# Performance work log

Hardware: AMD Instinct MI355X
Metric: run time of the kernel (lower is better)

The kernel has to match this reference:

```python
import jax, jax.numpy as jnp
import numpy as np


def setup_inputs() -> dict:
    key = jax.random.key(0)
    k1, k2 = jax.random.split(key)
    N, C, H, W = 32, 1, 768, 1024
    inp = jax.random.normal(k1, (N, C, H, W), dtype=jnp.float32)
    # target values in {0,1,2}: 0=neg, 1=pos, 2=ignore
    tgt = jax.random.randint(k2, (N, C, H, W), 0, 3).astype(jnp.float32)
    return {"input": inp, "target": tgt}


def reference(input, target):
    # Flatten (NCHW -> NHWC -> flat); order is irrelevant for a mean reduction,
    # but we mirror the original transpose/view for faithfulness.
    x = jnp.transpose(input, (0, 2, 3, 1)).reshape(-1)
    t = jnp.transpose(target, (0, 2, 3, 1)).reshape(-1)

    pos = t == 1.0
    neg = t == 0.0
    pos_num = jnp.sum(pos).astype(x.dtype)
    neg_num = jnp.sum(neg).astype(x.dtype)
    sum_num = pos_num + neg_num

    # weight: neg_num/sum for positives, pos_num/sum for negatives, 0 for ignore (t>1)
    w = jnp.where(pos, neg_num / sum_num, jnp.where(neg, pos_num / sum_num, 0.0))

    # stable BCE-with-logits: max(x,0) - x*t + log1p(exp(-|x|))
    bce = jnp.maximum(x, 0.0) - x * t + jnp.log1p(jnp.exp(-jnp.abs(x)))
    return jnp.mean(w * bce)
```

## Files before the change

kernel.cpp:

```cpp
#include <hip/hip_runtime.h>


#define GRID1 2048
#define BLOCK 256

__device__ __forceinline__ void do_elem(float xv, float tv,
                                        float& cp, float& cn,
                                        float& sp, float& sn) {
  float a = fabsf(xv);
  float e = __expf(-a);
  float l = __logf(1.0f + e);
  float c = fmaxf(xv, 0.f) + l;
  bool pos = (tv == 1.0f);
  bool neg = (tv == 0.0f);
  cp += pos ? 1.0f : 0.0f;
  cn += neg ? 1.0f : 0.0f;
  sp += pos ? (c - xv) : 0.0f;
  sn += neg ? c : 0.0f;
}

__device__ __forceinline__ void do_vec4(float4 xv, float4 tv,
                                        float& cp, float& cn,
                                        float& sp, float& sn) {
  do_elem(xv.x, tv.x, cp, cn, sp, sn);
  do_elem(xv.y, tv.y, cp, cn, sp, sn);
  do_elem(xv.z, tv.z, cp, cn, sp, sn);
  do_elem(xv.w, tv.w, cp, cn, sp, sn);
}

__global__ __launch_bounds__(BLOCK, 8) void edge_loss_stage1(
    const float* __restrict__ x, const float* __restrict__ t,
    float* __restrict__ partials, long long n) {
  long long tid = (long long)blockIdx.x * BLOCK + threadIdx.x;
  long long S = (long long)gridDim.x * BLOCK;
  long long n4 = n >> 2;

  float cp = 0.f, cn = 0.f, sp = 0.f, sn = 0.f;

  const float4* __restrict__ x4 = (const float4*)x;
  const float4* __restrict__ t4 = (const float4*)t;

  long long i = tid;
  if (i < n4) {
    float4 xa = x4[i];
    float4 ta = t4[i];
    long long nxt = i + S;
    while (nxt < n4) {
      float4 xb = x4[nxt];
      float4 tb = t4[nxt];
      do_vec4(xa, ta, cp, cn, sp, sn);
      xa = xb;
      ta = tb;
      nxt += S;
    }
    do_vec4(xa, ta, cp, cn, sp, sn);
  }
  for (long long j = (n4 << 2) + tid; j < n; j += S) {
    do_elem(x[j], t[j], cp, cn, sp, sn);
  }

  #pragma unroll
  for (int off = 32; off > 0; off >>= 1) {
    cp += __shfl_down(cp, off, 64);
    cn += __shfl_down(cn, off, 64);
    sp += __shfl_down(sp, off, 64);
    sn += __shfl_down(sn, off, 64);
  }

  __shared__ float s_cp[4], s_cn[4], s_sp[4], s_sn[4];
  int lane = threadIdx.x & 63;
  int wave = threadIdx.x >> 6;
  if (lane == 0) { s_cp[wave] = cp; s_cn[wave] = cn; s_sp[wave] = sp; s_sn[wave] = sn; }
  __syncthreads();
  if (threadIdx.x == 0) {
    float tcp = 0.f, tcn = 0.f, tsp = 0.f, tsn = 0.f;
    #pragma unroll
    for (int k = 0; k < 4; ++k) { tcp += s_cp[k]; tcn += s_cn[k]; tsp += s_sp[k]; tsn += s_sn[k]; }
    int G = gridDim.x;
    partials[0 * G + blockIdx.x] = tcp;
    partials[1 * G + blockIdx.x] = tcn;
    partials[2 * G + blockIdx.x] = tsp;
    partials[3 * G + blockIdx.x] = tsn;
  }
}

__global__ __launch_bounds__(BLOCK) void edge_loss_stage2(
    const float* __restrict__ partials, float* __restrict__ out,
    int G, double inv_n) {
  double acc[4] = {0.0, 0.0, 0.0, 0.0};
  for (int i = threadIdx.x; i < G; i += BLOCK) {
    #pragma unroll
    for (int c = 0; c < 4; ++c) acc[c] += (double)partials[c * G + i];
  }
  #pragma unroll
  for (int off = 32; off > 0; off >>= 1) {
    #pragma unroll
    for (int c = 0; c < 4; ++c) acc[c] += __shfl_down(acc[c], off, 64);
  }
  __shared__ double s_acc[4][4];
  int lane = threadIdx.x & 63;
  int wave = threadIdx.x >> 6;
  if (lane == 0) {
    #pragma unroll
    for (int c = 0; c < 4; ++c) s_acc[wave][c] = acc[c];
  }
  __syncthreads();
  if (threadIdx.x == 0) {
    double pos = 0, neg = 0, spos = 0, sneg = 0;
    #pragma unroll
    for (int w = 0; w < 4; ++w) {
      pos += s_acc[w][0]; neg += s_acc[w][1];
      spos += s_acc[w][2]; sneg += s_acc[w][3];
    }
    double s = pos + neg;
    out[0] = (float)((neg * spos + pos * sneg) / s * inv_n);
  }
}

extern "C" void kernel_launch(void* const* d_in, const int* in_sizes, int n_in,
                              void* d_out, int out_size, void* d_ws, size_t ws_size,
                              hipStream_t stream) {
  const float* x = (const float*)d_in[0];
  const float* t = (const float*)d_in[1];
  long long n = (long long)in_sizes[0];
  float* partials = (float*)d_ws;

  edge_loss_stage1<<<GRID1, BLOCK, 0, stream>>>(x, t, partials, n);
  edge_loss_stage2<<<1, BLOCK, 0, stream>>>(partials, (float*)d_out,
                                            GRID1, 1.0 / (double)n);
}
```

Measured before the change: 215.0 us.

## Stream inputs through LDS with async global_load_lds double buffering

The register-prefetch grid-stride loop is replaced by direct global-to-LDS DMA loads (global_load_lds, 16 bytes per lane) into a per-wave double buffer, with s_waitcnt on vmcnt gating each stage. The goal is to keep loads in flight without holding them in VGPRs and so hide memory latency in this bandwidth-bound reduction. It adds LDS traffic, 16 KB of shared memory per block that may limit occupancy, and relies on hand-coded waitcnt encodings whose correctness depends on the target ISA.

Measured after the change: 216.8 us. Within noise of the previous version (+0.8%).

```diff
diff --git a/kernel.cpp b/kernel.cpp
--- a/kernel.cpp
+++ b/kernel.cpp
@@ -3,6 +3,15 @@
 
 #define GRID1 2048
 #define BLOCK 256
+
+#define WAITCNT_VM2 0x0F72
+#define WAITCNT_VM0 0x0F70
+
+__device__ __forceinline__ void dma16(const float4* g, float4* l) {
+  __builtin_amdgcn_global_load_lds(
+      (const __attribute__((address_space(1))) void*)g,
+      (__attribute__((address_space(3))) void*)l, 16, 0, 0);
+}
 
 __device__ __forceinline__ void do_elem(float xv, float tv,
                                         float& cp, float& cn,
@@ -31,31 +40,52 @@
 __global__ __launch_bounds__(BLOCK, 8) void edge_loss_stage1(
     const float* __restrict__ x, const float* __restrict__ t,
     float* __restrict__ partials, long long n) {
-  long long tid = (long long)blockIdx.x * BLOCK + threadIdx.x;
+  __shared__ float4 lds[2][2][BLOCK];
+
+  long long idx0 = (long long)blockIdx.x * BLOCK + threadIdx.x;
   long long S = (long long)gridDim.x * BLOCK;
   long long n4 = n >> 2;
+  long long niter = n4 / S;
 
-  float cp = 0.f, cn = 0.f, sp = 0.f, sn = 0.f;
+  int lane = threadIdx.x & 63;
+  int wave = threadIdx.x >> 6;
 
   const float4* __restrict__ x4 = (const float4*)x;
   const float4* __restrict__ t4 = (const float4*)t;
 
-  long long i = tid;
-  if (i < n4) {
-    float4 xa = x4[i];
-    float4 ta = t4[i];
-    long long nxt = i + S;
-    while (nxt < n4) {
-      float4 xb = x4[nxt];
-      float4 tb = t4[nxt];
-      do_vec4(xa, ta, cp, cn, sp, sn);
-      xa = xb;
-      ta = tb;
-      nxt += S;
+  float cp = 0.f, cn = 0.f, sp = 0.f, sn = 0.f;
+
+  float4* lx0 = &lds[0][0][wave * 64];
+  float4* lt0 = &lds[0][1][wave * 64];
+  float4* lx1 = &lds[1][0][wave * 64];
+  float4* lt1 = &lds[1][1][wave * 64];
+
+  long long g = idx0;
+  if (niter > 0) {
+    dma16(x4 + g, lx0);
+    dma16(t4 + g, lt0);
+  }
+  #pragma unroll 1
+  for (long long k = 0; k < niter; ++k) {
+    int cur = (int)(k & 1);
+    if (k + 1 < niter) {
+      long long gn = g + S;
+      dma16(x4 + gn, cur ? lx0 : lx1);
+      dma16(t4 + gn, cur ? lt0 : lt1);
+      __builtin_amdgcn_s_waitcnt(WAITCNT_VM2);
+    } else {
+      __builtin_amdgcn_s_waitcnt(WAITCNT_VM0);
     }
-    do_vec4(xa, ta, cp, cn, sp, sn);
+    __asm__ volatile("" ::: "memory");
+    float4 xv = (cur ? lx1 : lx0)[lane];
+    float4 tv = (cur ? lt1 : lt0)[lane];
+    do_vec4(xv, tv, cp, cn, sp, sn);
+    g += S;
   }
-  for (long long j = (n4 << 2) + tid; j < n; j += S) {
+  if (g < n4) {
+    do_vec4(x4[g], t4[g], cp, cn, sp, sn);
+  }
+  for (long long j = (n4 << 2) + idx0; j < n; j += S) {
     do_elem(x[j], t[j], cp, cn, sp, sn);
   }
 
@@ -68,8 +98,6 @@
   }
 
   __shared__ float s_cp[4], s_cn[4], s_sp[4], s_sn[4];
-  int lane = threadIdx.x & 63;
-  int wave = threadIdx.x >> 6;
   if (lane == 0) { s_cp[wave] = cp; s_cn[wave] = cn; s_sp[wave] = sp; s_sn[wave] = sn; }
   __syncthreads();
   if (threadIdx.x == 0) {
```
